# Optimization experiments

Measured on AMD Instinct MI355X. Metric: run time of the kernel, lower is better.

Reference implementation:

```python
import jax, jax.numpy as jnp
import numpy as np

# FUME epipolar image translation: for each output pixel p2=(x2,y2) the fundamental
# matrix F maps it to a line l = F @ [x2*d, y2*d, 1] in the input view (full-res
# coordinates; d = per-batch downsampling factor). The output value is the line
# integral of the input image along that epipolar line, computed by stepping one
# pixel at a time along the dominant axis with bilinear (1-D linear) interpolation
# across the other axis; out-of-bounds samples contribute zero.

def _translate(img, F, d):
    B, C, H, W = img.shape
    dt = img.dtype
    yy, xx = jnp.meshgrid(jnp.arange(H, dtype=dt), jnp.arange(W, dtype=dt), indexing='ij')
    db = d[:, None, None].astype(dt)                          # (B,1,1)
    px, py = xx[None] * db, yy[None] * db                     # (B,H,W) full-res coords
    a = F[0, 0] * px + F[0, 1] * py + F[0, 2]                 # line coeffs l = F @ [x,y,1]
    b = F[1, 0] * px + F[1, 1] * py + F[1, 2]
    c = F[2, 0] * px + F[2, 1] * py + F[2, 2]
    horiz = jnp.abs(b) >= jnp.abs(a)                          # dominant axis per pixel

    db4 = db[..., None]                                       # (B,1,1,1)
    # horizontal traversal: step over columns s, solve a*(s*d) + b*(y*d) + c = 0
    s = jnp.arange(W, dtype=dt)
    denom_h = jnp.where(horiz, b, jnp.ones((), dt))[..., None] * db4
    yline = -(a[..., None] * (s * db4) + c[..., None]) / denom_h    # (B,H,W,W)
    # vertical traversal: step over rows t, solve for x
    t = jnp.arange(H, dtype=dt)
    denom_v = jnp.where(horiz, jnp.ones((), dt), a)[..., None] * db4
    xline = -(b[..., None] * (t * db4) + c[..., None]) / denom_v    # (B,H,W,H)

    def sample_one(imgb, y, x):
        # imgb: (C,H,W); y: (H,W,W) row coord per column step; x: (H,W,H) col coord per row step
        y0 = jnp.floor(y)
        wy = y - y0
        y0i = jnp.clip(y0.astype(jnp.int32), 0, H - 1)
        y1i = jnp.clip(y0i + 1, 0, H - 1)
        cols = jnp.arange(W)
        vh = (1 - wy)[None] * imgb[:, y0i, cols] + wy[None] * imgb[:, y1i, cols]  # (C,H,W,W)
        vh = jnp.where(((y >= 0) & (y <= H - 1))[None], vh, jnp.zeros((), imgb.dtype)).sum(-1)

        x0 = jnp.floor(x)
        wx = x - x0
        x0i = jnp.clip(x0.astype(jnp.int32), 0, W - 1)
        x1i = jnp.clip(x0i + 1, 0, W - 1)
        rows = jnp.arange(H)
        vv = (1 - wx)[None] * imgb[:, rows, x0i] + wx[None] * imgb[:, rows, x1i]  # (C,H,W,H)
        vv = jnp.where(((x >= 0) & (x <= W - 1))[None], vv, jnp.zeros((), imgb.dtype)).sum(-1)
        return vh, vv

    vh, vv = jax.vmap(sample_one)(img, yline, xline)          # each (B,C,H,W)
    return jnp.where(horiz[:, None], vh, vv)


def setup_inputs() -> dict:
    key = jax.random.key(0)
    k1, k2, k3 = jax.random.split(key, 3)
    B, C, H, W = 4, 4, 128, 128
    view1 = jax.random.normal(k1, (B, C, H, W), jnp.float32)
    F21 = jax.random.normal(k2, (3, 3), jnp.float32)
    F12 = jax.random.normal(k3, (3, 3), jnp.float32)
    downsampled_factor = jnp.ones((B,), jnp.float32)
    return {"view1": view1, "F21": F21, "F12": F12, "downsampled_factor": downsampled_factor}


def reference(view1, F21, F12, downsampled_factor):
    # forward uses F21 only; F12 is kept for the backward pass in the original module
    return _translate(view1, F21, downsampled_factor)
```

## Files before the change

### kernel.cpp

```cpp
#include <hip/hip_runtime.h>


#define CC 4
#define HH 128
#define WW 128
#define LDK 128
#define CUBE (128 * LDK)

typedef _Float16 h2 __attribute__((ext_vector_type(2)));

__global__ void __launch_bounds__(128) fume_stage(
        const float* __restrict__ img, float4* __restrict__ ws) {
    int t   = threadIdx.x;
    int u   = blockIdx.x;
    int dir = blockIdx.y;
    int b   = blockIdx.z;
    const float* src = img + (size_t)b * CC * HH * WW;
    float4* base = ws + (size_t)b * (2 * CUBE) + (dir ? CUBE : 0);
    int u1 = min(u + 1, HH - 1);

    h2 p0, p1, p2, p3;
    if (dir == 0) {
        p0 = (h2){ (_Float16)src[(0 * HH + u) * WW + t], (_Float16)src[(0 * HH + u1) * WW + t] };
        p1 = (h2){ (_Float16)src[(1 * HH + u) * WW + t], (_Float16)src[(1 * HH + u1) * WW + t] };
        p2 = (h2){ (_Float16)src[(2 * HH + u) * WW + t], (_Float16)src[(2 * HH + u1) * WW + t] };
        p3 = (h2){ (_Float16)src[(3 * HH + u) * WW + t], (_Float16)src[(3 * HH + u1) * WW + t] };
    } else {
        p0 = (h2){ (_Float16)src[(0 * HH + t) * WW + u], (_Float16)src[(0 * HH + t) * WW + u1] };
        p1 = (h2){ (_Float16)src[(1 * HH + t) * WW + u], (_Float16)src[(1 * HH + t) * WW + u1] };
        p2 = (h2){ (_Float16)src[(2 * HH + t) * WW + u], (_Float16)src[(2 * HH + t) * WW + u1] };
        p3 = (h2){ (_Float16)src[(3 * HH + t) * WW + u], (_Float16)src[(3 * HH + t) * WW + u1] };
    }
    base[u * LDK + t] = make_float4(__builtin_bit_cast(float, p0),
                                    __builtin_bit_cast(float, p1),
                                    __builtin_bit_cast(float, p2),
                                    __builtin_bit_cast(float, p3));
}

__global__ void __launch_bounds__(512) fume_kernel(
        const float4* __restrict__ cubes,
        const float* __restrict__ F,
        const float* __restrict__ dsf,
        float* __restrict__ out) {
    int tx  = threadIdx.x;
    int seg = threadIdx.y;
    int x = blockIdx.x * 64 + tx;
    int y = blockIdx.y;
    int b = blockIdx.z;

    float d = dsf[b];
    float F00 = F[0], F01 = F[1], F02 = F[2];
    float F10 = F[3], F11 = F[4], F12 = F[5];
    float F20 = F[6], F21 = F[7], F22 = F[8];

    float px = __fmul_rn((float)x, d);
    float py = __fmul_rn((float)y, d);
    float av = __fadd_rn(__fadd_rn(__fmul_rn(F00, px), __fmul_rn(F01, py)), F02);
    float bv = __fadd_rn(__fadd_rn(__fmul_rn(F10, px), __fmul_rn(F11, py)), F12);
    float cv = __fadd_rn(__fadd_rn(__fmul_rn(F20, px), __fmul_rn(F21, py)), F22);

    bool horiz  = fabsf(bv) >= fabsf(av);
    float ncoef = horiz ? av : bv;
    float den   = __fmul_rn(horiz ? bv : av, d);
    float nrec  = -__fdiv_rn(1.0f, den);

    const float4* P = cubes + (size_t)b * (2 * CUBE) + (horiz ? 0 : CUBE);

    float A  = __fmul_rn(__fmul_rn(ncoef, d), nrec);
    float Bc = __fmul_rn(cv, nrec);
    int lkmin, lkmax;
    if (fabsf(A) > 1e-20f) {
        float inv = 1.0f / A;
        float k1 = (0.0f   - Bc) * inv;
        float k2 = (127.0f - Bc) * inv;
        float lo = fmaxf(fminf(k1, k2) - 2.0f, 0.0f);
        float hi = fminf(fmaxf(k1, k2) + 2.0f, 127.0f);
        if (lo > hi || !(lo == lo)) { lkmin = 1; lkmax = 0; }
        else { lkmin = (int)lo; lkmax = (int)hi; }
    } else {
        bool full = (Bc >= 0.0f) && (Bc <= 127.0f);
        lkmin = full ? 0 : 1;
        lkmax = full ? 127 : 0;
    }

    float a0 = 0.f, a1 = 0.f, a2 = 0.f, a3 = 0.f;
    int len = lkmax - lkmin + 1;
    int cnt = (len + 7) >> 3;
    int ks  = lkmin + seg * cnt;
    int ke  = min(ks + cnt - 1, lkmax);
    #pragma unroll 8
    for (int k = ks; k <= ke; ++k) {
        float m  = __fmul_rn((float)k, d);
        float q  = __fadd_rn(__fmul_rn(ncoef, m), cv);
        float u  = __fmul_rn(q, nrec);
        bool ok  = (u >= 0.f) && (u <= 127.f);
        int i0   = (int)floorf(u);
        i0 = max(0, min(i0, 126));
        float w  = __fsub_rn(u, (float)i0);
        h2 wp = __builtin_bit_cast(h2,
                    __builtin_amdgcn_cvt_pkrtz(__fsub_rn(1.f, w), w));
        wp = ok ? wp : (h2){(_Float16)0.f, (_Float16)0.f};
        float4 e = P[i0 * LDK + k];
        a0 = __builtin_amdgcn_fdot2(wp, __builtin_bit_cast(h2, e.x), a0, false);
        a1 = __builtin_amdgcn_fdot2(wp, __builtin_bit_cast(h2, e.y), a1, false);
        a2 = __builtin_amdgcn_fdot2(wp, __builtin_bit_cast(h2, e.z), a2, false);
        a3 = __builtin_amdgcn_fdot2(wp, __builtin_bit_cast(h2, e.w), a3, false);
    }

    __shared__ float part[8][4][64];
    part[seg][0][tx] = a0;
    part[seg][1][tx] = a1;
    part[seg][2][tx] = a2;
    part[seg][3][tx] = a3;
    __syncthreads();

    if (seg < 4) {
        int ch = seg;
        float s = part[0][ch][tx];
        #pragma unroll
        for (int t = 1; t < 8; ++t) s = __fadd_rn(s, part[t][ch][tx]);
        out[(((size_t)b * CC + ch) * HH + y) * WW + x] = s;
    }
}

extern "C" void kernel_launch(void* const* d_in, const int* in_sizes, int n_in,
                              void* d_out, int out_size, void* d_ws, size_t ws_size,
                              hipStream_t stream) {
    const float* view1 = (const float*)d_in[0];
    const float* F21   = (const float*)d_in[1];
    const float* dsf   = (const float*)d_in[3];

    const int B = in_sizes[3];

    dim3 stb(128, 1, 1);
    dim3 stg(HH, 2, B);
    fume_stage<<<stg, stb, 0, stream>>>(view1, (float4*)d_ws);

    dim3 ftb(64, 8, 1);
    dim3 ftg(WW / 64, HH, B);
    fume_kernel<<<ftg, ftb, 0, stream>>>((const float4*)d_ws, F21, dsf,
                                         (float*)d_out);
}
```

Measured before the change: 69.69 us.

## Fuse staging and sampling kernels into one cooperative launch with grid sync

Merges the fp16 staging kernel and the line-integral kernel into a single cooperative kernel. Each thread first writes one staged workspace entry, then the whole grid synchronizes before sampling. Each block now handles a full output row (two 64-wide halves) instead of half a row. This removes one kernel launch and the gap between launches, at the cost of a grid-wide barrier, the cooperative-launch overhead and half as many blocks in the main phase.

```diff
diff --git a/kernel.cpp b/kernel.cpp
--- a/kernel.cpp
+++ b/kernel.cpp
@@ -1,4 +1,7 @@
 #include <hip/hip_runtime.h>
+#include <hip/hip_cooperative_groups.h>
+
+namespace cg = cooperative_groups;
 
 
 #define CC 4
@@ -9,117 +12,133 @@
 
 typedef _Float16 h2 __attribute__((ext_vector_type(2)));
 
-__global__ void __launch_bounds__(128) fume_stage(
-        const float* __restrict__ img, float4* __restrict__ ws) {
-    int t   = threadIdx.x;
-    int u   = blockIdx.x;
-    int dir = blockIdx.y;
-    int b   = blockIdx.z;
-    const float* src = img + (size_t)b * CC * HH * WW;
-    float4* base = ws + (size_t)b * (2 * CUBE) + (dir ? CUBE : 0);
-    int u1 = min(u + 1, HH - 1);
-
-    h2 p0, p1, p2, p3;
-    if (dir == 0) {
-        p0 = (h2){ (_Float16)src[(0 * HH + u) * WW + t], (_Float16)src[(0 * HH + u1) * WW + t] };
-        p1 = (h2){ (_Float16)src[(1 * HH + u) * WW + t], (_Float16)src[(1 * HH + u1) * WW + t] };
-        p2 = (h2){ (_Float16)src[(2 * HH + u) * WW + t], (_Float16)src[(2 * HH + u1) * WW + t] };
-        p3 = (h2){ (_Float16)src[(3 * HH + u) * WW + t], (_Float16)src[(3 * HH + u1) * WW + t] };
-    } else {
-        p0 = (h2){ (_Float16)src[(0 * HH + t) * WW + u], (_Float16)src[(0 * HH + t) * WW + u1] };
-        p1 = (h2){ (_Float16)src[(1 * HH + t) * WW + u], (_Float16)src[(1 * HH + t) * WW + u1] };
-        p2 = (h2){ (_Float16)src[(2 * HH + t) * WW + u], (_Float16)src[(2 * HH + t) * WW + u1] };
-        p3 = (h2){ (_Float16)src[(3 * HH + t) * WW + u], (_Float16)src[(3 * HH + t) * WW + u1] };
-    }
-    base[u * LDK + t] = make_float4(__builtin_bit_cast(float, p0),
-                                    __builtin_bit_cast(float, p1),
-                                    __builtin_bit_cast(float, p2),
-                                    __builtin_bit_cast(float, p3));
-}
-
-__global__ void __launch_bounds__(512) fume_kernel(
-        const float4* __restrict__ cubes,
+__global__ void __launch_bounds__(512, 4) fume_fused(
+        float4* __restrict__ ws,
+        const float* __restrict__ img,
         const float* __restrict__ F,
         const float* __restrict__ dsf,
-        float* __restrict__ out) {
+        float* __restrict__ out,
+        int B) {
     int tx  = threadIdx.x;
     int seg = threadIdx.y;
-    int x = blockIdx.x * 64 + tx;
-    int y = blockIdx.y;
-    int b = blockIdx.z;
+    int bid = blockIdx.x;
+
+    {
+        int gtid = bid * 512 + seg * 64 + tx;
+        int nent = B << 15;
+        if (gtid < nent) {
+            int b   = gtid >> 15;
+            int r   = gtid & 32767;
+            int dir = r >> 14;
+            int rr  = r & 16383;
+            int u   = rr >> 7;
+            int t   = rr & 127;
+            const float* src = img + (size_t)b * CC * HH * WW;
+            int u1 = min(u + 1, HH - 1);
+            h2 p0, p1, p2, p3;
+            if (dir == 0) {
+                p0 = (h2){ (_Float16)src[(0 * HH + u) * WW + t], (_Float16)src[(0 * HH + u1) * WW + t] };
+                p1 = (h2){ (_Float16)src[(1 * HH + u) * WW + t], (_Float16)src[(1 * HH + u1) * WW + t] };
+                p2 = (h2){ (_Float16)src[(2 * HH + u) * WW + t], (_Float16)src[(2 * HH + u1) * WW + t] };
+                p3 = (h2){ (_Float16)src[(3 * HH + u) * WW + t], (_Float16)src[(3 * HH + u1) * WW + t] };
+            } else {
+                p0 = (h2){ (_Float16)src[(0 * HH + t) * WW + u], (_Float16)src[(0 * HH + t) * WW + u1] };
+                p1 = (h2){ (_Float16)src[(1 * HH + t) * WW + u], (_Float16)src[(1 * HH + t) * WW + u1] };
+                p2 = (h2){ (_Float16)src[(2 * HH + t) * WW + u], (_Float16)src[(2 * HH + t) * WW + u1] };
+                p3 = (h2){ (_Float16)src[(3 * HH + t) * WW + u], (_Float16)src[(3 * HH + t) * WW + u1] };
+            }
+            ws[((size_t)b * 2 + dir) * CUBE + u * LDK + t] =
+                make_float4(__builtin_bit_cast(float, p0),
+                            __builtin_bit_cast(float, p1),
+                            __builtin_bit_cast(float, p2),
+                            __builtin_bit_cast(float, p3));
+        }
+    }
+    __threadfence();
+    cg::this_grid().sync();
+
+    int y = bid & 127;
+    int b = bid >> 7;
 
     float d = dsf[b];
     float F00 = F[0], F01 = F[1], F02 = F[2];
     float F10 = F[3], F11 = F[4], F12 = F[5];
     float F20 = F[6], F21 = F[7], F22 = F[8];
 
-    float px = __fmul_rn((float)x, d);
-    float py = __fmul_rn((float)y, d);
-    float av = __fadd_rn(__fadd_rn(__fmul_rn(F00, px), __fmul_rn(F01, py)), F02);
-    float bv = __fadd_rn(__fadd_rn(__fmul_rn(F10, px), __fmul_rn(F11, py)), F12);
-    float cv = __fadd_rn(__fadd_rn(__fmul_rn(F20, px), __fmul_rn(F21, py)), F22);
+    const float4* cb = ws + (size_t)b * (2 * CUBE);
+    __shared__ float part[8][4][64];
 
-    bool horiz  = fabsf(bv) >= fabsf(av);
-    float ncoef = horiz ? av : bv;
-    float den   = __fmul_rn(horiz ? bv : av, d);
-    float nrec  = -__fdiv_rn(1.0f, den);
+    for (int xh = 0; xh < 2; ++xh) {
+        int x = xh * 64 + tx;
 
-    const float4* P = cubes + (size_t)b * (2 * CUBE) + (horiz ? 0 : CUBE);
+        float px = __fmul_rn((float)x, d);
+        float py = __fmul_rn((float)y, d);
+        float av = __fadd_rn(__fadd_rn(__fmul_rn(F00, px), __fmul_rn(F01, py)), F02);
+        float bv = __fadd_rn(__fadd_rn(__fmul_rn(F10, px), __fmul_rn(F11, py)), F12);
+        float cv = __fadd_rn(__fadd_rn(__fmul_rn(F20, px), __fmul_rn(F21, py)), F22);
 
-    float A  = __fmul_rn(__fmul_rn(ncoef, d), nrec);
-    float Bc = __fmul_rn(cv, nrec);
-    int lkmin, lkmax;
-    if (fabsf(A) > 1e-20f) {
-        float inv = 1.0f / A;
-        float k1 = (0.0f   - Bc) * inv;
-        float k2 = (127.0f - Bc) * inv;
-        float lo = fmaxf(fminf(k1, k2) - 2.0f, 0.0f);
-        float hi = fminf(fmaxf(k1, k2) + 2.0f, 127.0f);
-        if (lo > hi || !(lo == lo)) { lkmin = 1; lkmax = 0; }
-        else { lkmin = (int)lo; lkmax = (int)hi; }
-    } else {
-        bool full = (Bc >= 0.0f) && (Bc <= 127.0f);
-        lkmin = full ? 0 : 1;
-        lkmax = full ? 127 : 0;
-    }
+        bool horiz  = fabsf(bv) >= fabsf(av);
+        float ncoef = horiz ? av : bv;
+        float den   = __fmul_rn(horiz ? bv : av, d);
+        float nrec  = -__fdiv_rn(1.0f, den);
 
-    float a0 = 0.f, a1 = 0.f, a2 = 0.f, a3 = 0.f;
-    int len = lkmax - lkmin + 1;
-    int cnt = (len + 7) >> 3;
-    int ks  = lkmin + seg * cnt;
-    int ke  = min(ks + cnt - 1, lkmax);
-    #pragma unroll 8
-    for (int k = ks; k <= ke; ++k) {
-        float m  = __fmul_rn((float)k, d);
-        float q  = __fadd_rn(__fmul_rn(ncoef, m), cv);
-        float u  = __fmul_rn(q, nrec);
-        bool ok  = (u >= 0.f) && (u <= 127.f);
-        int i0   = (int)floorf(u);
-        i0 = max(0, min(i0, 126));
-        float w  = __fsub_rn(u, (float)i0);
-        h2 wp = __builtin_bit_cast(h2,
-                    __builtin_amdgcn_cvt_pkrtz(__fsub_rn(1.f, w), w));
-        wp = ok ? wp : (h2){(_Float16)0.f, (_Float16)0.f};
-        float4 e = P[i0 * LDK + k];
-        a0 = __builtin_amdgcn_fdot2(wp, __builtin_bit_cast(h2, e.x), a0, false);
-        a1 = __builtin_amdgcn_fdot2(wp, __builtin_bit_cast(h2, e.y), a1, false);
-        a2 = __builtin_amdgcn_fdot2(wp, __builtin_bit_cast(h2, e.z), a2, false);
-        a3 = __builtin_amdgcn_fdot2(wp, __builtin_bit_cast(h2, e.w), a3, false);
-    }
+        const float4* P = cb + (horiz ? 0 : CUBE);
 
-    __shared__ float part[8][4][64];
-    part[seg][0][tx] = a0;
-    part[seg][1][tx] = a1;
-    part[seg][2][tx] = a2;
-    part[seg][3][tx] = a3;
-    __syncthreads();
+        float A  = __fmul_rn(__fmul_rn(ncoef, d), nrec);
+        float Bc = __fmul_rn(cv, nrec);
+        int lkmin, lkmax;
+        if (fabsf(A) > 1e-20f) {
+            float inv = 1.0f / A;
+            float k1 = (0.0f   - Bc) * inv;
+            float k2 = (127.0f - Bc) * inv;
+            float lo = fmaxf(fminf(k1, k2) - 2.0f, 0.0f);
+            float hi = fminf(fmaxf(k1, k2) + 2.0f, 127.0f);
+            if (lo > hi || !(lo == lo)) { lkmin = 1; lkmax = 0; }
+            else { lkmin = (int)lo; lkmax = (int)hi; }
+        } else {
+            bool full = (Bc >= 0.0f) && (Bc <= 127.0f);
+            lkmin = full ? 0 : 1;
+            lkmax = full ? 127 : 0;
+        }
 
-    if (seg < 4) {
-        int ch = seg;
-        float s = part[0][ch][tx];
-        #pragma unroll
-        for (int t = 1; t < 8; ++t) s = __fadd_rn(s, part[t][ch][tx]);
-        out[(((size_t)b * CC + ch) * HH + y) * WW + x] = s;
+        float a0 = 0.f, a1 = 0.f, a2 = 0.f, a3 = 0.f;
+        int len = lkmax - lkmin + 1;
+        int cnt = (len + 7) >> 3;
+        int ks  = lkmin + seg * cnt;
+        int ke  = min(ks + cnt - 1, lkmax);
+        #pragma unroll 8
+        for (int k = ks; k <= ke; ++k) {
+            float m  = __fmul_rn((float)k, d);
+            float q  = __fadd_rn(__fmul_rn(ncoef, m), cv);
+            float u  = __fmul_rn(q, nrec);
+            bool ok  = (u >= 0.f) && (u <= 127.f);
+            int i0   = (int)floorf(u);
+            i0 = max(0, min(i0, 126));
+            float w  = __fsub_rn(u, (float)i0);
+            h2 wp = __builtin_bit_cast(h2,
+                        __builtin_amdgcn_cvt_pkrtz(__fsub_rn(1.f, w), w));
+            wp = ok ? wp : (h2){(_Float16)0.f, (_Float16)0.f};
+            float4 e = P[i0 * LDK + k];
+            a0 = __builtin_amdgcn_fdot2(wp, __builtin_bit_cast(h2, e.x), a0, false);
+            a1 = __builtin_amdgcn_fdot2(wp, __builtin_bit_cast(h2, e.y), a1, false);
+            a2 = __builtin_amdgcn_fdot2(wp, __builtin_bit_cast(h2, e.z), a2, false);
+            a3 = __builtin_amdgcn_fdot2(wp, __builtin_bit_cast(h2, e.w), a3, false);
+        }
+
+        part[seg][0][tx] = a0;
+        part[seg][1][tx] = a1;
+        part[seg][2][tx] = a2;
+        part[seg][3][tx] = a3;
+        __syncthreads();
+
+        if (seg < 4) {
+            int ch = seg;
+            float s = part[0][ch][tx];
+            #pragma unroll
+            for (int t = 1; t < 8; ++t) s = __fadd_rn(s, part[t][ch][tx]);
+            out[(((size_t)b * CC + ch) * HH + y) * WW + x] = s;
+        }
+        __syncthreads();
     }
 }
 
@@ -129,15 +148,14 @@
     const float* view1 = (const float*)d_in[0];
     const float* F21   = (const float*)d_in[1];
     const float* dsf   = (const float*)d_in[3];
+    float* outp        = (float*)d_out;
+    float4* ws         = (float4*)d_ws;
 
-    const int B = in_sizes[3];
+    int B = in_sizes[3];
 
-    dim3 stb(128, 1, 1);
-    dim3 stg(HH, 2, B);
-    fume_stage<<<stg, stb, 0, stream>>>(view1, (float4*)d_ws);
-
-    dim3 ftb(64, 8, 1);
-    dim3 ftg(WW / 64, HH, B);
-    fume_kernel<<<ftg, ftb, 0, stream>>>((const float4*)d_ws, F21, dsf,
-                                         (float*)d_out);
+    void* args[] = { (void*)&ws, (void*)&view1, (void*)&F21, (void*)&dsf,
+                     (void*)&outp, (void*)&B };
+    hipLaunchCooperativeKernel((void*)fume_fused,
+                               dim3(128 * B, 1, 1), dim3(64, 8, 1),
+                               args, 0, stream);
 }
```

New measurement: 212.7 us. +205.2%, slower.

## Drop staging kernel and gather fp32 image samples directly in main kernel

Applied to the files above, without the earlier changes.

Removes the pre-pass that packed neighbouring rows/columns of all four channels into fp16 float4 cubes, and instead has the main kernel read eight scattered fp32 values from the original image per step. This saves one kernel launch and the workspace write/read round trip. In exchange, each step now issues eight scalar gathers instead of one 16-byte load. The loop unroll is also reduced from 8 to 4.

```diff
diff --git a/kernel.cpp b/kernel.cpp
--- a/kernel.cpp
+++ b/kernel.cpp
@@ -4,41 +4,12 @@
 #define CC 4
 #define HH 128
 #define WW 128
-#define LDK 128
-#define CUBE (128 * LDK)
+#define HW (HH * WW)
 
 typedef _Float16 h2 __attribute__((ext_vector_type(2)));
 
-__global__ void __launch_bounds__(128) fume_stage(
-        const float* __restrict__ img, float4* __restrict__ ws) {
-    int t   = threadIdx.x;
-    int u   = blockIdx.x;
-    int dir = blockIdx.y;
-    int b   = blockIdx.z;
-    const float* src = img + (size_t)b * CC * HH * WW;
-    float4* base = ws + (size_t)b * (2 * CUBE) + (dir ? CUBE : 0);
-    int u1 = min(u + 1, HH - 1);
-
-    h2 p0, p1, p2, p3;
-    if (dir == 0) {
-        p0 = (h2){ (_Float16)src[(0 * HH + u) * WW + t], (_Float16)src[(0 * HH + u1) * WW + t] };
-        p1 = (h2){ (_Float16)src[(1 * HH + u) * WW + t], (_Float16)src[(1 * HH + u1) * WW + t] };
-        p2 = (h2){ (_Float16)src[(2 * HH + u) * WW + t], (_Float16)src[(2 * HH + u1) * WW + t] };
-        p3 = (h2){ (_Float16)src[(3 * HH + u) * WW + t], (_Float16)src[(3 * HH + u1) * WW + t] };
-    } else {
-        p0 = (h2){ (_Float16)src[(0 * HH + t) * WW + u], (_Float16)src[(0 * HH + t) * WW + u1] };
-        p1 = (h2){ (_Float16)src[(1 * HH + t) * WW + u], (_Float16)src[(1 * HH + t) * WW + u1] };
-        p2 = (h2){ (_Float16)src[(2 * HH + t) * WW + u], (_Float16)src[(2 * HH + t) * WW + u1] };
-        p3 = (h2){ (_Float16)src[(3 * HH + t) * WW + u], (_Float16)src[(3 * HH + t) * WW + u1] };
-    }
-    base[u * LDK + t] = make_float4(__builtin_bit_cast(float, p0),
-                                    __builtin_bit_cast(float, p1),
-                                    __builtin_bit_cast(float, p2),
-                                    __builtin_bit_cast(float, p3));
-}
-
 __global__ void __launch_bounds__(512) fume_kernel(
-        const float4* __restrict__ cubes,
+        const float* __restrict__ img,
         const float* __restrict__ F,
         const float* __restrict__ dsf,
         float* __restrict__ out) {
@@ -64,7 +35,7 @@
     float den   = __fmul_rn(horiz ? bv : av, d);
     float nrec  = -__fdiv_rn(1.0f, den);
 
-    const float4* P = cubes + (size_t)b * (2 * CUBE) + (horiz ? 0 : CUBE);
+    const float* sb = img + (size_t)b * CC * HW;
 
     float A  = __fmul_rn(__fmul_rn(ncoef, d), nrec);
     float Bc = __fmul_rn(cv, nrec);
@@ -83,12 +54,14 @@
         lkmax = full ? 127 : 0;
     }
 
+    int ostep = horiz ? WW : 1;
+
     float a0 = 0.f, a1 = 0.f, a2 = 0.f, a3 = 0.f;
     int len = lkmax - lkmin + 1;
     int cnt = (len + 7) >> 3;
     int ks  = lkmin + seg * cnt;
     int ke  = min(ks + cnt - 1, lkmax);
-    #pragma unroll 8
+    #pragma unroll 4
     for (int k = ks; k <= ke; ++k) {
         float m  = __fmul_rn((float)k, d);
         float q  = __fadd_rn(__fmul_rn(ncoef, m), cv);
@@ -100,11 +73,18 @@
         h2 wp = __builtin_bit_cast(h2,
                     __builtin_amdgcn_cvt_pkrtz(__fsub_rn(1.f, w), w));
         wp = ok ? wp : (h2){(_Float16)0.f, (_Float16)0.f};
-        float4 e = P[i0 * LDK + k];
-        a0 = __builtin_amdgcn_fdot2(wp, __builtin_bit_cast(h2, e.x), a0, false);
-        a1 = __builtin_amdgcn_fdot2(wp, __builtin_bit_cast(h2, e.y), a1, false);
-        a2 = __builtin_amdgcn_fdot2(wp, __builtin_bit_cast(h2, e.z), a2, false);
-        a3 = __builtin_amdgcn_fdot2(wp, __builtin_bit_cast(h2, e.w), a3, false);
+        int o0 = horiz ? (i0 * WW + k) : (k * WW + i0);
+        int o1 = o0 + ostep;
+        {
+            h2 e0 = { (_Float16)sb[0 * HW + o0], (_Float16)sb[0 * HW + o1] };
+            h2 e1 = { (_Float16)sb[1 * HW + o0], (_Float16)sb[1 * HW + o1] };
+            h2 e2 = { (_Float16)sb[2 * HW + o0], (_Float16)sb[2 * HW + o1] };
+            h2 e3 = { (_Float16)sb[3 * HW + o0], (_Float16)sb[3 * HW + o1] };
+            a0 = __builtin_amdgcn_fdot2(wp, e0, a0, false);
+            a1 = __builtin_amdgcn_fdot2(wp, e1, a1, false);
+            a2 = __builtin_amdgcn_fdot2(wp, e2, a2, false);
+            a3 = __builtin_amdgcn_fdot2(wp, e3, a3, false);
+        }
     }
 
     __shared__ float part[8][4][64];
@@ -132,12 +112,7 @@
 
     const int B = in_sizes[3];
 
-    dim3 stb(128, 1, 1);
-    dim3 stg(HH, 2, B);
-    fume_stage<<<stg, stb, 0, stream>>>(view1, (float4*)d_ws);
-
     dim3 ftb(64, 8, 1);
     dim3 ftg(WW / 64, HH, B);
-    fume_kernel<<<ftg, ftb, 0, stream>>>((const float4*)d_ws, F21, dsf,
-                                         (float*)d_out);
+    fume_kernel<<<ftg, ftb, 0, stream>>>(view1, F21, dsf, (float*)d_out);
 }
```

New measurement: 81.45 us. +16.9%, slower.
